# Kernel tuning notes

Hardware: AMD Instinct MI355X
Metric: run time of the kernel (lower is better)

The kernel has to match this reference:

```python
import jax, jax.numpy as jnp
import numpy as np

N = 50000          # nodes
DEG = 16           # graph_max_neighbor
E = N * DEG        # edges (sorted by receiver)
DIM = 128          # config.hidden_dimension
EDGE_DIM = 32
EPS = 1e-5


def _ln(x, scale, offset, mask):
    # masked LayerNorm over last axis: normalize per row, then apply node mask
    m = jnp.mean(x, axis=-1, keepdims=True)
    v = jnp.mean(jnp.square(x - m), axis=-1, keepdims=True)
    return ((x - m) * jax.lax.rsqrt(v + EPS) * scale + offset) * mask


def setup_inputs() -> dict:
    key = jax.random.key(0)
    ks = jax.random.split(key, 12)
    node_inp = jax.random.normal(ks[0], (N, DIM), jnp.float32)
    edge_feat = jax.random.normal(ks[1], (E, EDGE_DIM), jnp.float32)
    node_mask = jnp.ones((N, 1), jnp.float32)
    senders = jax.random.randint(ks[2], (E,), 0, N, jnp.int32)
    receivers = jnp.repeat(jnp.arange(N, dtype=jnp.int32), DEG)  # sorted, DEG per node
    din_e = 2 * DIM + EDGE_DIM
    s = lambda d: 1.0 / np.sqrt(d)
    We1 = jax.random.normal(ks[3], (din_e, 2 * DIM), jnp.float32) * s(din_e)
    be1 = jnp.zeros((2 * DIM,), jnp.float32)
    We2 = jax.random.normal(ks[4], (2 * DIM, DIM), jnp.float32) * s(2 * DIM)
    be2 = jnp.zeros((DIM,), jnp.float32)
    g_msg = jnp.ones((DIM,), jnp.float32)
    b_msg = jnp.zeros((DIM,), jnp.float32)
    Wn1 = jax.random.normal(ks[5], (2 * DIM, 2 * DIM), jnp.float32) * s(2 * DIM)
    bn1 = jnp.zeros((2 * DIM,), jnp.float32)
    Wn2 = jax.random.normal(ks[6], (2 * DIM, DIM), jnp.float32) * s(2 * DIM)
    bn2 = jnp.zeros((DIM,), jnp.float32)
    g_node = jnp.ones((DIM,), jnp.float32)
    b_node = jnp.zeros((DIM,), jnp.float32)
    return dict(node_inp=node_inp, edge_feat=edge_feat, node_mask=node_mask,
                We1=We1, be1=be1, We2=We2, be2=be2, g_msg=g_msg, b_msg=b_msg,
                Wn1=Wn1, bn1=bn1, Wn2=Wn2, bn2=bn2, g_node=g_node, b_node=b_node,
                senders=senders, receivers=receivers)


def reference(node_inp, edge_feat, node_mask, We1, be1, We2, be2, g_msg, b_msg,
              Wn1, bn1, Wn2, bn2, g_node, b_node, senders, receivers):
    # gather + concat -> edge MLP (swish, no final activation; haiku MLP default)
    msg_input = jnp.concatenate(
        [node_inp[senders], node_inp[receivers], edge_feat], axis=-1)  # [E, 2*DIM+EDGE_DIM]
    h = jax.nn.swish(msg_input @ We1 + be1)
    messages = h @ We2 + be2                                           # [E, DIM]
    # scatter-reduce to receivers (sorted), mean over max neighbors
    agg = jax.ops.segment_sum(messages, receivers, num_segments=node_inp.shape[0],
                              indices_are_sorted=True) / DEG
    agg = _ln(agg, g_msg, b_msg, node_mask)
    # node update MLP + residual + masked LN
    nf = jnp.concatenate([node_inp, agg], axis=-1)                     # [N, 2*DIM]
    nf = jax.nn.swish(nf @ Wn1 + bn1) @ Wn2 + bn2                      # [N, DIM]
    nf = node_inp + nf
    return _ln(nf, g_node, b_node, node_mask)
```

## Files before the change

kernel.cpp:

```cpp
#include <hip/hip_runtime.h>

typedef _Float16 F16;
typedef _Float16 half8 __attribute__((ext_vector_type(8)));
typedef _Float16 half2 __attribute__((ext_vector_type(2)));
typedef float f32x4 __attribute__((ext_vector_type(4)));

#define N_NODES 50000
#define DEG 16
#define N_EDGES (N_NODES * DEG)
#define DIM 128

__device__ __forceinline__ float frcp(float x) { float r; asm("v_rcp_f32 %0, %1" : "=v"(r) : "v"(x)); return r; }
__device__ __forceinline__ float frsq(float x) { float r; asm("v_rsq_f32 %0, %1" : "=v"(r) : "v"(x)); return r; }
__device__ __forceinline__ float fexp2(float x) { float r; asm("v_exp_f32 %0, %1" : "=v"(r) : "v"(x)); return r; }
__device__ __forceinline__ float swishf(float x) { return x * frcp(1.0f + fexp2(x * -1.442695041f)); }

__device__ __forceinline__ half8 cvt8(f32x4 a, f32x4 b) {
    half8 h; h[0]=(F16)a[0]; h[1]=(F16)a[1]; h[2]=(F16)a[2]; h[3]=(F16)a[3];
    h[4]=(F16)b[0]; h[5]=(F16)b[1]; h[6]=(F16)b[2]; h[7]=(F16)b[3]; return h;
}

__device__ __forceinline__ void pack_one(const float* src, F16* dst, int idx,
                                         int K, int NC, int ld, int row0, int split) {
    int j = idx & 7;
    int l = (idx >> 3) & 63;
    int blob = idx >> 9;
    int ntiles = NC >> 4;
    int tcol = blob % ntiles;
    int c = blob / ntiles;
    int k = c * 32 + ((l >> 4) * 8) + j;
    int col = tcol * 16 + (l & 15);
    int sr = row0 + k, sc = col;
    if (split && col >= split) { sr += K; sc -= split; }
    dst[idx] = (F16)src[(size_t)sr * ld + sc];
}

__global__ void k_pack_all(const float* __restrict__ We1, const float* __restrict__ We2,
                           const float* __restrict__ Wn1, const float* __restrict__ Wn2,
                           F16* w1abp, F16* w1ep, F16* we2p, F16* wn1p, F16* wn2p) {
    int b = blockIdx.x, t = threadIdx.x;
    if (b < 256)      pack_one(We1, w1abp, (b - 0)   * 256 + t, 128, 512, 256, 0,   256);
    else if (b < 288) pack_one(We1, w1ep,  (b - 256) * 256 + t, 32,  256, 256, 256, 0);
    else if (b < 416) pack_one(We2, we2p,  (b - 288) * 256 + t, 256, 128, 128, 0,   0);
    else if (b < 672) pack_one(Wn1, wn1p,  (b - 416) * 256 + t, 256, 256, 256, 0,   0);
    else              pack_one(Wn2, wn2p,  (b - 672) * 256 + t, 256, 128, 128, 0,   0);
}

#define PAS 152
__global__ __launch_bounds__(256, 2) void k_proj(
    const float* __restrict__ node_inp, const float* __restrict__ be1,
    const F16* __restrict__ w1abp, F16* __restrict__ Ps, F16* __restrict__ Pr)
{
    __shared__ __align__(16) F16 A[64 * PAS];
    const int t = threadIdx.x;
    const int n0 = blockIdx.x * 64;

    #pragma unroll
    for (int i = 0; i < 4; ++i) {
        int id = t + i * 256; int row = id >> 4, c = id & 15;
        int gn = n0 + row; if (gn >= N_NODES) gn = N_NODES - 1;
        f32x4 v0 = *(const f32x4*)(node_inp + (size_t)gn * DIM + c * 8);
        f32x4 v1 = *(const f32x4*)(node_inp + (size_t)gn * DIM + c * 8 + 4);
        *(half8*)&A[row * PAS + c * 8] = cvt8(v0, v1);
    }
    __syncthreads();

    const int lane = t & 63, wn = t >> 6;
    const int lcol = lane & 15, quad = lane >> 4;

    f32x4 acc[4][8] = {};
    #pragma unroll
    for (int c = 0; c < 4; ++c) {
        half8 af[4];
        #pragma unroll
        for (int rt = 0; rt < 4; ++rt)
            af[rt] = *(const half8*)&A[(rt * 16 + lcol) * PAS + c * 32 + quad * 8];
        const F16* wp = w1abp + (((size_t)(c * 32 + wn * 8)) * 64 + lane) * 8;
        #pragma unroll
        for (int nt = 0; nt < 8; ++nt) {
            half8 bv = *(const half8*)(wp + (size_t)nt * 512);
            #pragma unroll
            for (int rt = 0; rt < 4; ++rt)
                acc[rt][nt] = __builtin_amdgcn_mfma_f32_16x16x32_f16(af[rt], bv, acc[rt][nt], 0, 0, 0);
        }
    }

    F16* dst = (wn < 2) ? Ps : Pr;
    const int cb = (wn & 1) * 128;
    #pragma unroll
    for (int nt = 0; nt < 8; ++nt) {
        int col = cb + nt * 16 + lcol;
        float bias = (wn >= 2) ? be1[col] : 0.0f;
        #pragma unroll
        for (int rt = 0; rt < 4; ++rt) {
            #pragma unroll
            for (int r = 0; r < 4; ++r) {
                int gn = n0 + rt * 16 + quad * 4 + r;
                if (gn < N_NODES) dst[(size_t)gn * 256 + col] = (F16)(acc[rt][nt][r] + bias);
            }
        }
    }
}

#define PGS2 136
__global__ __launch_bounds__(256, 4) void k_edge(
    const F16* __restrict__ Ps, const F16* Pr,
    const float* __restrict__ edge_feat, const int* __restrict__ senders,
    const F16* __restrict__ w1ep, F16* Hm)
{
    __shared__ __align__(16) F16 Pg[4 * 16 * PGS2];
    __shared__ int sidx[64];
    const int t = threadIdx.x;
    const int n0 = blockIdx.x * 4;
    const int e0 = n0 * 16;
    const int lane = t & 63, nd = t >> 6;
    const int lcol = lane & 15, quad = lane >> 4;
    const int n = n0 + nd;

    if (t < 64) sidx[t] = senders[e0 + t];

    f32x4 v0 = *(const f32x4*)(edge_feat + (size_t)(e0 + nd * 16 + lcol) * 32 + quad * 8);
    f32x4 v1 = *(const f32x4*)(edge_feat + (size_t)(e0 + nd * 16 + lcol) * 32 + quad * 8 + 4);
    half8 a = cvt8(v0, v1);
    __syncthreads();

    F16* pg = &Pg[nd * 16 * PGS2];
    #pragma unroll
    for (int h = 0; h < 2; ++h) {
        #pragma unroll
        for (int i = 0; i < 4; ++i) {
            int id = lane + i * 64; int row = id >> 4, c = id & 15;
            int s = sidx[nd * 16 + row];
            half8 ps = *(const half8*)(Ps + (size_t)s * 256 + h * 128 + c * 8);
            half8 pr = *(const half8*)(Pr + (size_t)n * 256 + h * 128 + c * 8);
            *(half8*)&pg[row * PGS2 + c * 8] = ps + pr;
        }
        f32x4 acc[8] = {};
        #pragma unroll
        for (int j = 0; j < 8; ++j) {
            half8 bv = *(const half8*)(w1ep + (((size_t)(h * 8 + j)) * 64 + lane) * 8);
            acc[j] = __builtin_amdgcn_mfma_f32_16x16x32_f16(a, bv, acc[j], 0, 0, 0);
        }
        #pragma unroll
        for (int j = 0; j < 8; ++j) {
            const F16* pgp = &pg[(quad * 4) * PGS2 + j * 16 + lcol];
            float s = 0.f;
            #pragma unroll
            for (int r = 0; r < 4; ++r) {
                float x = acc[j][r] + (float)pgp[r * PGS2];
                s += swishf(x);
            }
            s += __shfl_xor(s, 16, 64);
            s += __shfl_xor(s, 32, 64);
            if (lane < 16) Hm[(size_t)n * 256 + h * 128 + j * 16 + lane] = (F16)(s * 0.0625f);
        }
    }
}

#define XS 280
#define FSS 139
__global__ __launch_bounds__(256, 4) void k_node(
    const float* __restrict__ node_inp, const F16* Hm,
    const float* __restrict__ be2, const float* __restrict__ g_msg, const float* __restrict__ b_msg,
    const float* __restrict__ bn1, const float* __restrict__ bn2,
    const float* __restrict__ g_node, const float* __restrict__ b_node,
    const float* __restrict__ node_mask,
    const F16* __restrict__ we2p, const F16* __restrict__ wn1p, const F16* __restrict__ wn2p,
    float* out)
{
    __shared__ __align__(16) unsigned char smem[64 * XS * 2];
    F16* X = (F16*)smem;
    float* Fs = (float*)smem;

    const int t = threadIdx.x;
    const int n0 = blockIdx.x * 64;
    const int lane = t & 63, w = t >> 6;
    const int lcol = lane & 15, quad = lane >> 4;

    #pragma unroll
    for (int i = 0; i < 4; ++i) {
        int id = t + i * 256; int row = id >> 4, c = id & 15;
        int gn = n0 + row; if (gn >= N_NODES) gn = N_NODES - 1;
        f32x4 v0 = *(const f32x4*)(node_inp + (size_t)gn * DIM + c * 8);
        f32x4 v1 = *(const f32x4*)(node_inp + (size_t)gn * DIM + c * 8 + 4);
        *(half8*)&X[row * XS + c * 8] = cvt8(v0, v1);
    }

    {
        const int r0 = w * 16;
        int gr = n0 + r0 + lcol; if (gr >= N_NODES) gr = N_NODES - 1;
        const F16* hrow = Hm + (size_t)gr * 256;
        f32x4 acc[8] = {};
        #pragma unroll
        for (int c = 0; c < 8; ++c) {
            half8 af = *(const half8*)(hrow + c * 32 + quad * 8);
            const F16* wp = we2p + (((size_t)(c * 8)) * 64 + lane) * 8;
            #pragma unroll
            for (int nt = 0; nt < 8; ++nt) {
                half8 bv = *(const half8*)(wp + (size_t)nt * 512);
                acc[nt] = __builtin_amdgcn_mfma_f32_16x16x32_f16(af, bv, acc[nt], 0, 0, 0);
            }
        }
        #pragma unroll
        for (int nt = 0; nt < 8; ++nt) {
            int col = nt * 16 + lcol;
            float b = be2[col];
            #pragma unroll
            for (int r = 0; r < 4; ++r)
                X[(r0 + quad * 4 + r) * XS + 128 + col] = (F16)(acc[nt][r] + b);
        }
    }
    __syncthreads();

    {
        int row = t >> 2, q = t & 3;
        int gn = n0 + row; if (gn >= N_NODES) gn = N_NODES - 1;
        float vv[32]; float sum = 0.f, sq = 0.f;
        #pragma unroll
        for (int j = 0; j < 4; ++j) {
            half8 hv = *(const half8*)&X[row * XS + 128 + q * 32 + j * 8];
            #pragma unroll
            for (int k = 0; k < 8; ++k) { float f = (float)hv[k]; vv[j*8+k] = f; sum += f; sq += f*f; }
        }
        sum += __shfl_xor(sum, 1, 64); sq += __shfl_xor(sq, 1, 64);
        sum += __shfl_xor(sum, 2, 64); sq += __shfl_xor(sq, 2, 64);
        float mean = sum * (1.0f / DIM);
        float rs = frsq(sq * (1.0f / DIM) - mean * mean + 1e-5f);
        float msk = node_mask[gn];
        #pragma unroll
        for (int j = 0; j < 16; ++j) {
            int col = q * 32 + j * 2;
            half2 o;
            o[0] = (F16)(((vv[j*2]   - mean) * rs * g_msg[col]   + b_msg[col])   * msk);
            o[1] = (F16)(((vv[j*2+1] - mean) * rs * g_msg[col+1] + b_msg[col+1]) * msk);
            *(half2*)&X[row * XS + 128 + col] = o;
        }
    }
    __syncthreads();

    {
        f32x4 acc1[4][4] = {};
        #pragma unroll
        for (int c = 0; c < 8; ++c) {
            half8 af[4];
            #pragma unroll
            for (int rt = 0; rt < 4; ++rt)
                af[rt] = *(const half8*)&X[(rt * 16 + lcol) * XS + c * 32 + quad * 8];
            const F16* wp = wn1p + (((size_t)(c * 16 + w * 4)) * 64 + lane) * 8;
            #pragma unroll
            for (int nt = 0; nt < 4; ++nt) {
                half8 bv = *(const half8*)(wp + (size_t)nt * 512);
                #pragma unroll
                for (int rt = 0; rt < 4; ++rt)
                    acc1[rt][nt] = __builtin_amdgcn_mfma_f32_16x16x32_f16(af[rt], bv, acc1[rt][nt], 0, 0, 0);
            }
        }
        __syncthreads();
        #pragma unroll
        for (int nt = 0; nt < 4; ++nt) {
            int col = w * 64 + nt * 16 + lcol;
            float b = bn1[col];
            #pragma unroll
            for (int rt = 0; rt < 4; ++rt)
                #pragma unroll
                for (int r = 0; r < 4; ++r) {
                    float x = acc1[rt][nt][r] + b;
                    X[(rt * 16 + quad * 4 + r) * XS + col] = (F16)swishf(x);
                }
        }
    }
    __syncthreads();

    {
        f32x4 acc2[4][2] = {};
        #pragma unroll
        for (int c = 0; c < 8; ++c) {
            half8 af[4];
            #pragma unroll
            for (int rt = 0; rt < 4; ++rt)
                af[rt] = *(const half8*)&X[(rt * 16 + lcol) * XS + c * 32 + quad * 8];
            const F16* wp = wn2p + (((size_t)(c * 8 + w * 2)) * 64 + lane) * 8;
            #pragma unroll
            for (int nt = 0; nt < 2; ++nt) {
                half8 bv = *(const half8*)(wp + (size_t)nt * 512);
                #pragma unroll
                for (int rt = 0; rt < 4; ++rt)
                    acc2[rt][nt] = __builtin_amdgcn_mfma_f32_16x16x32_f16(af[rt], bv, acc2[rt][nt], 0, 0, 0);
            }
        }
        __syncthreads();
        #pragma unroll
        for (int nt = 0; nt < 2; ++nt) {
            int col = w * 32 + nt * 16 + lcol;
            float b = bn2[col];
            #pragma unroll
            for (int rt = 0; rt < 4; ++rt)
                #pragma unroll
                for (int r = 0; r < 4; ++r)
                    Fs[(rt * 16 + quad * 4 + r) * FSS + col] = acc2[rt][nt][r] + b;
        }
    }
    __syncthreads();

    {
        int row = t >> 2, q = t & 3;
        int gn = n0 + row;
        f32x4 xr[8];
        float sum = 0.f, sq = 0.f;
        if (gn < N_NODES) {
            #pragma unroll
            for (int j = 0; j < 8; ++j) {
                f32x4 aa = *(const f32x4*)&Fs[row * FSS + q * 32 + j * 4];
                f32x4 ni = *(const f32x4*)(node_inp + (size_t)gn * DIM + q * 32 + j * 4);
                f32x4 x = aa + ni;
                xr[j] = x;
                sum += x[0] + x[1] + x[2] + x[3];
                sq  += x[0]*x[0] + x[1]*x[1] + x[2]*x[2] + x[3]*x[3];
            }
        }
        sum += __shfl_xor(sum, 1, 64); sq += __shfl_xor(sq, 1, 64);
        sum += __shfl_xor(sum, 2, 64); sq += __shfl_xor(sq, 2, 64);
        if (gn < N_NODES) {
            float mean = sum * (1.0f / DIM);
            float rs = frsq(sq * (1.0f / DIM) - mean * mean + 1e-5f);
            float msk = node_mask[gn];
            #pragma unroll
            for (int j = 0; j < 8; ++j) {
                f32x4 o;
                #pragma unroll
                for (int qq = 0; qq < 4; ++qq) {
                    int col = q * 32 + j * 4 + qq;
                    o[qq] = ((xr[j][qq] - mean) * rs * g_node[col] + b_node[col]) * msk;
                }
                *(f32x4*)(out + (size_t)gn * DIM + q * 32 + j * 4) = o;
            }
        }
    }
}


extern "C" void kernel_launch(void* const* d_in, const int* in_sizes, int n_in,
                              void* d_out, int out_size, void* d_ws, size_t ws_size,
                              hipStream_t stream)
{
    const float* node_inp  = (const float*)d_in[0];
    const float* edge_feat = (const float*)d_in[1];
    const float* node_mask = (const float*)d_in[2];
    const float* We1 = (const float*)d_in[3];
    const float* be1 = (const float*)d_in[4];
    const float* We2 = (const float*)d_in[5];
    const float* be2 = (const float*)d_in[6];
    const float* g_msg = (const float*)d_in[7];
    const float* b_msg = (const float*)d_in[8];
    const float* Wn1 = (const float*)d_in[9];
    const float* bn1 = (const float*)d_in[10];
    const float* Wn2 = (const float*)d_in[11];
    const float* bn2 = (const float*)d_in[12];
    const float* g_node = (const float*)d_in[13];
    const float* b_node = (const float*)d_in[14];
    const int* senders = (const int*)d_in[15];
    float* out = (float*)d_out;

    char* ws = (char*)d_ws;
    F16* Ps = (F16*)ws;
    size_t off = (size_t)N_NODES * 256 * 2;
    F16* w1abp = (F16*)(ws + off); off += 128 * 512 * 2;
    F16* w1ep  = (F16*)(ws + off); off += 32 * 256 * 2;
    F16* we2p  = (F16*)(ws + off); off += 256 * 128 * 2;
    F16* wn1p  = (F16*)(ws + off); off += 256 * 256 * 2;
    F16* wn2p  = (F16*)(ws + off); off += 256 * 128 * 2;

    F16* PrHm = (F16*)d_out;

    k_pack_all<<<dim3(800), dim3(256), 0, stream>>>(We1, We2, Wn1, Wn2,
                                                    w1abp, w1ep, we2p, wn1p, wn2p);

    k_proj<<<dim3((N_NODES + 63) / 64), dim3(256), 0, stream>>>(node_inp, be1, w1abp, Ps, PrHm);

    k_edge<<<dim3(N_NODES / 4), dim3(256), 0, stream>>>(Ps, PrHm, edge_feat, senders, w1ep, PrHm);

    k_node<<<dim3((N_NODES + 63) / 64), dim3(256), 0, stream>>>(
        node_inp, PrHm, be2, g_msg, b_msg, bn1, bn2, g_node, b_node, node_mask,
        we2p, wn1p, wn2p, out);
}
```

Before: 362.8 us.

## Fold weight packing into projection kernel, split proj accumulators, fuse message LayerNorm

Most weight packing now runs as extra blocks of the projection kernel, and only the W1ab pack stays in its own launch. The projection kernel processes its columns in two halves to cut accumulator registers, and its launch bound rises to allow 4 blocks per CU. The edge kernel's launch bound rises to 8. In the node kernel, the message LayerNorm is computed directly from the MFMA accumulators with cross-lane shuffles, which removes a shared-memory round trip and one barrier. The tighter launch bounds risk register spills.

```diff
diff --git a/kernel.cpp b/kernel.cpp
--- a/kernel.cpp
+++ b/kernel.cpp
@@ -9,6 +9,7 @@
 #define DEG 16
 #define N_EDGES (N_NODES * DEG)
 #define DIM 128
+#define NPROJ 782
 
 __device__ __forceinline__ float frcp(float x) { float r; asm("v_rcp_f32 %0, %1" : "=v"(r) : "v"(x)); return r; }
 __device__ __forceinline__ float frsq(float x) { float r; asm("v_rsq_f32 %0, %1" : "=v"(r) : "v"(x)); return r; }
@@ -35,26 +36,32 @@
     dst[idx] = (F16)src[(size_t)sr * ld + sc];
 }
 
-__global__ void k_pack_all(const float* __restrict__ We1, const float* __restrict__ We2,
-                           const float* __restrict__ Wn1, const float* __restrict__ Wn2,
-                           F16* w1abp, F16* w1ep, F16* we2p, F16* wn1p, F16* wn2p) {
-    int b = blockIdx.x, t = threadIdx.x;
-    if (b < 256)      pack_one(We1, w1abp, (b - 0)   * 256 + t, 128, 512, 256, 0,   256);
-    else if (b < 288) pack_one(We1, w1ep,  (b - 256) * 256 + t, 32,  256, 256, 256, 0);
-    else if (b < 416) pack_one(We2, we2p,  (b - 288) * 256 + t, 256, 128, 128, 0,   0);
-    else if (b < 672) pack_one(Wn1, wn1p,  (b - 416) * 256 + t, 256, 256, 256, 0,   0);
-    else              pack_one(Wn2, wn2p,  (b - 672) * 256 + t, 256, 128, 128, 0,   0);
+__global__ void k_pack_w1ab(const float* __restrict__ We1, F16* w1abp) {
+    pack_one(We1, w1abp, blockIdx.x * 256 + threadIdx.x, 128, 512, 256, 0, 256);
 }
 
 #define PAS 152
-__global__ __launch_bounds__(256, 2) void k_proj(
+__global__ __launch_bounds__(256, 4) void k_proj_pack(
     const float* __restrict__ node_inp, const float* __restrict__ be1,
-    const F16* __restrict__ w1abp, F16* __restrict__ Ps, F16* __restrict__ Pr)
+    const F16* __restrict__ w1abp, F16* __restrict__ Ps, F16* __restrict__ Pr,
+    const float* __restrict__ We1, const float* __restrict__ We2,
+    const float* __restrict__ Wn1, const float* __restrict__ Wn2,
+    F16* w1ep, F16* we2p, F16* wn1p, F16* wn2p)
 {
     __shared__ __align__(16) F16 A[64 * PAS];
+    const int b = blockIdx.x;
     const int t = threadIdx.x;
-    const int n0 = blockIdx.x * 64;
-
+
+    if (b >= NPROJ) {
+        int b2 = b - NPROJ;
+        if (b2 < 32)       pack_one(We1, w1ep, b2 * 256 + t,        32, 256, 256, 256, 0);
+        else if (b2 < 160) pack_one(We2, we2p, (b2 - 32) * 256 + t, 256, 128, 128, 0, 0);
+        else if (b2 < 416) pack_one(Wn1, wn1p, (b2 - 160) * 256 + t, 256, 256, 256, 0, 0);
+        else               pack_one(Wn2, wn2p, (b2 - 416) * 256 + t, 256, 128, 128, 0, 0);
+        return;
+    }
+
+    const int n0 = b * 64;
     #pragma unroll
     for (int i = 0; i < 4; ++i) {
         int id = t + i * 256; int row = id >> 4, c = id & 15;
@@ -65,45 +72,46 @@
     }
     __syncthreads();
 
-    const int lane = t & 63, wn = t >> 6;
+    const int lane = t & 63, w = t >> 6;
     const int lcol = lane & 15, quad = lane >> 4;
-
-    f32x4 acc[4][8] = {};
+    F16* dst = (w < 2) ? Ps : Pr;
+    const int cb = (w & 1) * 128;
+
     #pragma unroll
-    for (int c = 0; c < 4; ++c) {
-        half8 af[4];
-        #pragma unroll
-        for (int rt = 0; rt < 4; ++rt)
-            af[rt] = *(const half8*)&A[(rt * 16 + lcol) * PAS + c * 32 + quad * 8];
-        const F16* wp = w1abp + (((size_t)(c * 32 + wn * 8)) * 64 + lane) * 8;
-        #pragma unroll
-        for (int nt = 0; nt < 8; ++nt) {
-            half8 bv = *(const half8*)(wp + (size_t)nt * 512);
-            #pragma unroll
-            for (int rt = 0; rt < 4; ++rt)
-                acc[rt][nt] = __builtin_amdgcn_mfma_f32_16x16x32_f16(af[rt], bv, acc[rt][nt], 0, 0, 0);
-        }
-    }
-
-    F16* dst = (wn < 2) ? Ps : Pr;
-    const int cb = (wn & 1) * 128;
-    #pragma unroll
-    for (int nt = 0; nt < 8; ++nt) {
-        int col = cb + nt * 16 + lcol;
-        float bias = (wn >= 2) ? be1[col] : 0.0f;
-        #pragma unroll
-        for (int rt = 0; rt < 4; ++rt) {
-            #pragma unroll
-            for (int r = 0; r < 4; ++r) {
-                int gn = n0 + rt * 16 + quad * 4 + r;
-                if (gn < N_NODES) dst[(size_t)gn * 256 + col] = (F16)(acc[rt][nt][r] + bias);
-            }
+    for (int p = 0; p < 2; ++p) {
+        f32x4 acc[4][4] = {};
+        #pragma unroll
+        for (int c = 0; c < 4; ++c) {
+            half8 af[4];
+            #pragma unroll
+            for (int rt = 0; rt < 4; ++rt)
+                af[rt] = *(const half8*)&A[(rt * 16 + lcol) * PAS + c * 32 + quad * 8];
+            const F16* wp = w1abp + (((size_t)(c * 32 + w * 8 + p * 4)) * 64 + lane) * 8;
+            #pragma unroll
+            for (int nt = 0; nt < 4; ++nt) {
+                half8 bv = *(const half8*)(wp + (size_t)nt * 512);
+                #pragma unroll
+                for (int rt = 0; rt < 4; ++rt)
+                    acc[rt][nt] = __builtin_amdgcn_mfma_f32_16x16x32_f16(af[rt], bv, acc[rt][nt], 0, 0, 0);
+            }
+        }
+        #pragma unroll
+        for (int nt = 0; nt < 4; ++nt) {
+            int col = cb + p * 64 + nt * 16 + lcol;
+            float bias = (w >= 2) ? be1[col] : 0.0f;
+            #pragma unroll
+            for (int rt = 0; rt < 4; ++rt)
+                #pragma unroll
+                for (int r = 0; r < 4; ++r) {
+                    int gn = n0 + rt * 16 + quad * 4 + r;
+                    if (gn < N_NODES) dst[(size_t)gn * 256 + col] = (F16)(acc[rt][nt][r] + bias);
+                }
         }
     }
 }
 
 #define PGS2 136
-__global__ __launch_bounds__(256, 4) void k_edge(
+__global__ __launch_bounds__(256, 8) void k_edge(
     const F16* __restrict__ Ps, const F16* Pr,
     const float* __restrict__ edge_feat, const int* __restrict__ senders,
     const F16* __restrict__ w1ep, F16* Hm)
@@ -176,18 +184,18 @@
     const int n0 = blockIdx.x * 64;
     const int lane = t & 63, w = t >> 6;
     const int lcol = lane & 15, quad = lane >> 4;
+    const int r0 = w * 16;
 
     #pragma unroll
     for (int i = 0; i < 4; ++i) {
         int id = t + i * 256; int row = id >> 4, c = id & 15;
         int gn = n0 + row; if (gn >= N_NODES) gn = N_NODES - 1;
-        f32x4 v0 = *(const f32x4*)(node_inp + (size_t)gn * DIM + c * 8);
-        f32x4 v1 = *(const f32x4*)(node_inp + (size_t)gn * DIM + c * 8 + 4);
-        *(half8*)&X[row * XS + c * 8] = cvt8(v0, v1);
+        f32x4 u0 = *(const f32x4*)(node_inp + (size_t)gn * DIM + c * 8);
+        f32x4 u1 = *(const f32x4*)(node_inp + (size_t)gn * DIM + c * 8 + 4);
+        *(half8*)&X[row * XS + c * 8] = cvt8(u0, u1);
     }
 
     {
-        const int r0 = w * 16;
         int gr = n0 + r0 + lcol; if (gr >= N_NODES) gr = N_NODES - 1;
         const F16* hrow = Hm + (size_t)gr * 256;
         f32x4 acc[8] = {};
@@ -201,39 +209,39 @@
                 acc[nt] = __builtin_amdgcn_mfma_f32_16x16x32_f16(af, bv, acc[nt], 0, 0, 0);
             }
         }
+        float sum[4] = {}, sq[4] = {};
+        #pragma unroll
+        for (int nt = 0; nt < 8; ++nt) {
+            float b = be2[nt * 16 + lcol];
+            #pragma unroll
+            for (int r = 0; r < 4; ++r) {
+                float v = acc[nt][r] + b;
+                acc[nt][r] = v; sum[r] += v; sq[r] += v * v;
+            }
+        }
+        #pragma unroll
+        for (int m = 1; m <= 8; m <<= 1)
+            #pragma unroll
+            for (int r = 0; r < 4; ++r) {
+                sum[r] += __shfl_xor(sum[r], m, 64);
+                sq[r]  += __shfl_xor(sq[r],  m, 64);
+            }
+        float mnv[4], rsv[4], mskv[4];
+        #pragma unroll
+        for (int r = 0; r < 4; ++r) {
+            int gn = n0 + r0 + quad * 4 + r; if (gn >= N_NODES) gn = N_NODES - 1;
+            mnv[r] = sum[r] * (1.0f / DIM);
+            rsv[r] = frsq(sq[r] * (1.0f / DIM) - mnv[r] * mnv[r] + 1e-5f);
+            mskv[r] = node_mask[gn];
+        }
         #pragma unroll
         for (int nt = 0; nt < 8; ++nt) {
             int col = nt * 16 + lcol;
-            float b = be2[col];
+            float gm = g_msg[col], bm = b_msg[col];
             #pragma unroll
             for (int r = 0; r < 4; ++r)
-                X[(r0 + quad * 4 + r) * XS + 128 + col] = (F16)(acc[nt][r] + b);
-        }
-    }
-    __syncthreads();
-
-    {
-        int row = t >> 2, q = t & 3;
-        int gn = n0 + row; if (gn >= N_NODES) gn = N_NODES - 1;
-        float vv[32]; float sum = 0.f, sq = 0.f;
-        #pragma unroll
-        for (int j = 0; j < 4; ++j) {
-            half8 hv = *(const half8*)&X[row * XS + 128 + q * 32 + j * 8];
-            #pragma unroll
-            for (int k = 0; k < 8; ++k) { float f = (float)hv[k]; vv[j*8+k] = f; sum += f; sq += f*f; }
-        }
-        sum += __shfl_xor(sum, 1, 64); sq += __shfl_xor(sq, 1, 64);
-        sum += __shfl_xor(sum, 2, 64); sq += __shfl_xor(sq, 2, 64);
-        float mean = sum * (1.0f / DIM);
-        float rs = frsq(sq * (1.0f / DIM) - mean * mean + 1e-5f);
-        float msk = node_mask[gn];
-        #pragma unroll
-        for (int j = 0; j < 16; ++j) {
-            int col = q * 32 + j * 2;
-            half2 o;
-            o[0] = (F16)(((vv[j*2]   - mean) * rs * g_msg[col]   + b_msg[col])   * msk);
-            o[1] = (F16)(((vv[j*2+1] - mean) * rs * g_msg[col+1] + b_msg[col+1]) * msk);
-            *(half2*)&X[row * XS + 128 + col] = o;
+                X[(r0 + quad * 4 + r) * XS + 128 + col] =
+                    (F16)(((acc[nt][r] - mnv[r]) * rsv[r] * gm + bm) * mskv[r]);
         }
     }
     __syncthreads();
@@ -372,12 +380,14 @@
 
     F16* PrHm = (F16*)d_out;
 
-    k_pack_all<<<dim3(800), dim3(256), 0, stream>>>(We1, We2, Wn1, Wn2,
-                                                    w1abp, w1ep, we2p, wn1p, wn2p);
-
-    k_proj<<<dim3((N_NODES + 63) / 64), dim3(256), 0, stream>>>(node_inp, be1, w1abp, Ps, PrHm);
-
-    k_edge<<<dim3(N_NODES / 4), dim3(256), 0, stream>>>(Ps, PrHm, edge_feat, senders, w1ep, PrHm);
+    k_pack_w1ab<<<dim3(256), dim3(256), 0, stream>>>(We1, w1abp);
+
+    k_proj_pack<<<dim3(NPROJ + 544), dim3(256), 0, stream>>>(
+        node_inp, be1, w1abp, Ps, PrHm,
+        We1, We2, Wn1, Wn2, w1ep, we2p, wn1p, wn2p);
+
+    k_edge<<<dim3(N_NODES / 4), dim3(256), 0, stream>>>(
+        Ps, PrHm, edge_feat, senders, w1ep, PrHm);
 
     k_node<<<dim3((N_NODES + 63) / 64), dim3(256), 0, stream>>>(
         node_inp, PrHm, be2, g_msg, b_msg, bn1, bn2, g_node, b_node, node_mask,
```

Result: slower. 451.5 us (+24.4%).
